# Kernel optimization log

Measured on AMD Instinct MI355X. Metric: run time of the kernel, lower is better.

## Reference

```python
import jax, jax.numpy as jnp
import numpy as np

TEMPERATURE = 0.07
ASYM_F = 1.5
ASYM_M = 0.5
N_F, N_M, D = 8192, 8192, 128


def setup_inputs() -> dict:
    key = jax.random.key(0)
    kf, km = jax.random.split(key)
    proj_f = jax.random.normal(kf, (N_F, D), dtype=jnp.float32)
    proj_m = jax.random.normal(km, (N_M, D), dtype=jnp.float32)
    # module expects L2-normalized projections
    proj_f = proj_f / jnp.linalg.norm(proj_f, axis=1, keepdims=True)
    proj_m = proj_m / jnp.linalg.norm(proj_m, axis=1, keepdims=True)
    return {"proj_f": proj_f, "proj_m": proj_m}


def _directional_loss(anchor, pos, temperature):
    # anchor: (Na, D), pos: (Np, D)
    sim_pos = jnp.einsum('ad,pd->ap', anchor, pos) / temperature        # (Na, Np)
    sim_neg = jnp.einsum('ad,bd->ab', anchor, anchor) / temperature    # (Na, Na)
    n = anchor.shape[0]
    eye = jnp.eye(n, dtype=bool)
    sim_neg = jnp.where(eye, -jnp.inf, sim_neg)  # mask self-similarity
    numerator = jax.nn.logsumexp(sim_pos, axis=1)
    # logsumexp over concat([sim_pos, sim_neg]) == logaddexp of row lses (no concat materialized)
    denominator = jnp.logaddexp(numerator, jax.nn.logsumexp(sim_neg, axis=1))
    return -jnp.mean(numerator - denominator)


def reference(proj_f, proj_m):
    loss_f2m = _directional_loss(proj_f, proj_m, TEMPERATURE)
    loss_m2f = _directional_loss(proj_m, proj_f, TEMPERATURE)
    return ASYM_F * loss_f2m + ASYM_M * loss_m2f
```

## Files before the change

### kernel.cpp

```cpp
#include <hip/hip_runtime.h>

#define NROWS 8192
#define KD    128
#define SQK1C 4.5398163f

typedef __bf16 bf16x8 __attribute__((ext_vector_type(8)));
typedef float  f32x4  __attribute__((ext_vector_type(4)));

typedef __attribute__((address_space(1))) void* gas_ptr;
typedef __attribute__((address_space(3))) void* las_ptr;

__device__ __forceinline__ unsigned short f2bf(float x) {
  unsigned int u = __builtin_bit_cast(unsigned int, x);
  unsigned int r = (u + 0x7FFFu + ((u >> 16) & 1u)) >> 16;
  return (unsigned short)r;
}

__global__ __launch_bounds__(256) void prep_kernel(const float4* __restrict__ F4,
                                                   const float4* __restrict__ M4,
                                                   ushort4* __restrict__ Fb4,
                                                   ushort4* __restrict__ Mb4,
                                                   float* __restrict__ sums) {
  int i = blockIdx.x * 256 + threadIdx.x;
  float4 f = F4[i];
  float4 m = M4[i];
  ushort4 fo, mo;
  fo.x = f2bf(f.x * SQK1C); fo.y = f2bf(f.y * SQK1C);
  fo.z = f2bf(f.z * SQK1C); fo.w = f2bf(f.w * SQK1C);
  mo.x = f2bf(m.x * SQK1C); mo.y = f2bf(m.y * SQK1C);
  mo.z = f2bf(m.z * SQK1C); mo.w = f2bf(m.w * SQK1C);
  Fb4[i] = fo;
  Mb4[i] = mo;
  if (i < 4 * NROWS) sums[i] = 0.0f;
}

__global__ __launch_bounds__(256, 3) void gemm_kernel(const unsigned short* __restrict__ Fb,
                                                      const unsigned short* __restrict__ Mb,
                                                      float* __restrict__ sums) {
  __shared__ __align__(16) unsigned short lds[2][64 * KD];

  const int bx = blockIdx.x;
  const int by = blockIdx.y;
  const int z  = blockIdx.z;

  const unsigned short* A;
  const unsigned short* B;
  float* rowsum;
  float* colsum = nullptr;
  if (z == 0)      { A = Fb; B = Mb; rowsum = sums;             colsum = sums + NROWS; }
  else if (z == 1) { A = Fb; B = Fb; rowsum = sums + 2 * NROWS; }
  else             { A = Mb; B = Mb; rowsum = sums + 3 * NROWS; }

  const int tid  = threadIdx.x;
  const int lane = tid & 63;
  const int wave = tid >> 6;
  const int wr = wave >> 1, wc = wave & 1;
  const int l15 = lane & 15, l4 = lane >> 4;

  auto stageB = [&](void* dst, const unsigned short* src) {
    #pragma unroll
    for (int i = 0; i < 4; ++i) {
      const int lin = tid * 16 + i * 4096;
      const int row = lin >> 8;
      const int sbc = (lin & 255) ^ ((row & 7) << 4);
      __builtin_amdgcn_global_load_lds((gas_ptr)((const char*)src + row * 256 + sbc),
                                       (las_ptr)((char*)dst + lin), 16, 0, 0);
    }
  };

  {
    const unsigned short* Abase = A + (size_t)by * 128 * KD;
    #pragma unroll
    for (int i = 0; i < 8; ++i) {
      const int lin = tid * 16 + i * 4096;
      const int row = lin >> 8;
      const int sbc = (lin & 255) ^ ((row & 7) << 4);
      __builtin_amdgcn_global_load_lds((gas_ptr)((const char*)Abase + row * 256 + sbc),
                                       (las_ptr)((char*)lds + lin), 16, 0, 0);
    }
  }
  __syncthreads();

  bf16x8 af[4][4];
  #pragma unroll
  for (int m = 0; m < 4; ++m) {
    const int row = wr * 64 + m * 16 + l15;
    const char* ab = (const char*)lds + row * 256;
    const int sw = (row & 7) << 4;
    #pragma unroll
    for (int k = 0; k < 4; ++k)
      af[m][k] = *(const bf16x8*)(ab + ((k * 64 + l4 * 16) ^ sw));
  }
  __syncthreads();

  float rowacc[16];
  #pragma unroll
  for (int i = 0; i < 16; ++i) rowacc[i] = 0.f;

  const unsigned short* Bbase = B + (size_t)bx * 1024 * KD;
  stageB(lds[0], Bbase);
  stageB(lds[1], Bbase + 64 * KD);
  __syncthreads();

  const int brow0 = wc * 32 + l15;
  const int bsw   = (brow0 & 7) << 4;

  for (int t = 0; t < 16; ++t) {
    const char* bb = (const char*)lds[t & 1];
    const char* pb0 = bb + brow0 * 256;

    f32x4 acc[4][2] = {};
    __builtin_amdgcn_s_setprio(1);
    #pragma unroll
    for (int k = 0; k < 4; ++k) {
      const int c = (k * 64 + l4 * 16) ^ bsw;
      bf16x8 b0 = *(const bf16x8*)(pb0 + c);
      bf16x8 b1 = *(const bf16x8*)(pb0 + 16 * 256 + c);
      #pragma unroll
      for (int m = 0; m < 4; ++m) {
        acc[m][0] = __builtin_amdgcn_mfma_f32_16x16x32_bf16(af[m][k], b0, acc[m][0], 0, 0, 0);
        acc[m][1] = __builtin_amdgcn_mfma_f32_16x16x32_bf16(af[m][k], b1, acc[m][1], 0, 0, 0);
      }
    }
    __builtin_amdgcn_s_setprio(0);

    const bool diag = (z > 0) && ((((bx << 4) + t) >> 1) == by);
    if (z == 0) {
      float ca0 = 0.f, ca1 = 0.f;
      #pragma unroll
      for (int m = 0; m < 4; ++m) {
        #pragma unroll
        for (int j = 0; j < 4; ++j) {
          float v0 = __builtin_amdgcn_exp2f(acc[m][0][j]);
          float v1 = __builtin_amdgcn_exp2f(acc[m][1][j]);
          rowacc[m * 4 + j] += v0 + v1;
          ca0 += v0; ca1 += v1;
        }
      }
      ca0 += __shfl_xor(ca0, 16);
      ca0 += __shfl_xor(ca0, 32);
      ca1 += __shfl_xor(ca1, 16);
      ca1 += __shfl_xor(ca1, 32);
      if (l4 == 0) {
        float* cp = colsum + bx * 1024 + t * 64 + wc * 32 + l15;
        unsafeAtomicAdd(cp, ca0);
        unsafeAtomicAdd(cp + 16, ca1);
      }
    } else {
      #pragma unroll
      for (int m = 0; m < 4; ++m) {
        #pragma unroll
        for (int j = 0; j < 4; ++j) {
          float v0 = __builtin_amdgcn_exp2f(acc[m][0][j]);
          float v1 = __builtin_amdgcn_exp2f(acc[m][1][j]);
          if (diag) {
            const int grow = by * 128 + wr * 64 + m * 16 + l4 * 4 + j;
            const int gcol = bx * 1024 + t * 64 + wc * 32 + l15;
            if (grow == gcol)      v0 = 0.f;
            if (grow == gcol + 16) v1 = 0.f;
          }
          rowacc[m * 4 + j] += v0 + v1;
        }
      }
    }
    __syncthreads();
    if (t < 14) stageB(lds[t & 1], Bbase + (size_t)(t + 2) * 64 * KD);
  }

  #pragma unroll
  for (int i = 0; i < 16; ++i) {
    float v = rowacc[i];
    v += __shfl_xor(v, 1);
    v += __shfl_xor(v, 2);
    v += __shfl_xor(v, 4);
    v += __shfl_xor(v, 8);
    rowacc[i] = v;
  }
  if (l15 == 0) {
    const int rbase = by * 128 + wr * 64 + l4 * 4;
    #pragma unroll
    for (int i = 0; i < 16; ++i)
      unsafeAtomicAdd(rowsum + rbase + (i >> 2) * 16 + (i & 3), rowacc[i]);
  }
}

__global__ __launch_bounds__(1024) void loss_kernel(const float* __restrict__ sums,
                                                    float* __restrict__ out) {
  const float* Spf = sums;
  const float* Spm = sums + NROWS;
  const float* Snf = sums + 2 * NROWS;
  const float* Snm = sums + 3 * NROWS;
  float accf = 0.f, accm = 0.f;
  for (int i = threadIdx.x; i < NROWS; i += 1024) {
    accf += log1pf(Snf[i] / Spf[i]);
    accm += log1pf(Snm[i] / Spm[i]);
  }
  float v = 1.5f * accf + 0.5f * accm;
  #pragma unroll
  for (int s = 1; s < 64; s <<= 1) v += __shfl_xor(v, s);
  __shared__ float red[16];
  if ((threadIdx.x & 63) == 0) red[threadIdx.x >> 6] = v;
  __syncthreads();
  if (threadIdx.x == 0) {
    float s = 0.f;
    #pragma unroll
    for (int i = 0; i < 16; ++i) s += red[i];
    out[0] = s * (1.0f / NROWS);
  }
}

extern "C" void kernel_launch(void* const* d_in, const int* in_sizes, int n_in,
                              void* d_out, int out_size, void* d_ws, size_t ws_size,
                              hipStream_t stream) {
  (void)in_sizes; (void)n_in; (void)out_size; (void)ws_size;
  const float* F = (const float*)d_in[0];
  const float* M = (const float*)d_in[1];
  float* out = (float*)d_out;

  float* sums = (float*)d_ws;
  unsigned short* Fb = (unsigned short*)((char*)d_ws + 4 * NROWS * sizeof(float));
  unsigned short* Mb = Fb + (size_t)NROWS * KD;

  prep_kernel<<<dim3(NROWS * KD / 4 / 256), dim3(256), 0, stream>>>(
      (const float4*)F, (const float4*)M, (ushort4*)Fb, (ushort4*)Mb, sums);
  gemm_kernel<<<dim3(8, 64, 3), dim3(256), 0, stream>>>(Fb, Mb, sums);
  loss_kernel<<<dim3(1), dim3(1024), 0, stream>>>(sums, out);
}
```

Baseline: 82.70 us.

## Replace direct global-to-LDS loads with register-staged prefetch pipeline

Swaps the global_load_lds path for ordinary global loads into registers that are then written to swizzled LDS, with loads issued one tile ahead of the LDS write to form a deeper prefetch. A fragments are now read directly from global memory into registers, which drops the initial LDS staging and one barrier. The first MFMA of each tile takes a zero accumulator instead of zero-initialising the array. This costs extra VGPRs for the staging registers, which may reduce occupancy at the declared 3 blocks per SM.

```diff
diff --git a/kernel.cpp b/kernel.cpp
--- a/kernel.cpp
+++ b/kernel.cpp
@@ -6,9 +6,6 @@
 
 typedef __bf16 bf16x8 __attribute__((ext_vector_type(8)));
 typedef float  f32x4  __attribute__((ext_vector_type(4)));
-
-typedef __attribute__((address_space(1))) void* gas_ptr;
-typedef __attribute__((address_space(3))) void* las_ptr;
 
 __device__ __forceinline__ unsigned short f2bf(float x) {
   unsigned int u = __builtin_bit_cast(unsigned int, x);
@@ -42,6 +39,7 @@
   const int bx = blockIdx.x;
   const int by = blockIdx.y;
   const int z  = blockIdx.z;
+  const int R  = by * 128;
 
   const unsigned short* A;
   const unsigned short* B;
@@ -57,59 +55,55 @@
   const int wr = wave >> 1, wc = wave & 1;
   const int l15 = lane & 15, l4 = lane >> 4;
 
-  auto stageB = [&](void* dst, const unsigned short* src) {
-    #pragma unroll
-    for (int i = 0; i < 4; ++i) {
-      const int lin = tid * 16 + i * 4096;
-      const int row = lin >> 8;
-      const int sbc = (lin & 255) ^ ((row & 7) << 4);
-      __builtin_amdgcn_global_load_lds((gas_ptr)((const char*)src + row * 256 + sbc),
-                                       (las_ptr)((char*)dst + lin), 16, 0, 0);
-    }
-  };
-
+  bf16x8 af[4][4];
   {
-    const unsigned short* Abase = A + (size_t)by * 128 * KD;
-    #pragma unroll
-    for (int i = 0; i < 8; ++i) {
-      const int lin = tid * 16 + i * 4096;
-      const int row = lin >> 8;
-      const int sbc = (lin & 255) ^ ((row & 7) << 4);
-      __builtin_amdgcn_global_load_lds((gas_ptr)((const char*)Abase + row * 256 + sbc),
-                                       (las_ptr)((char*)lds + lin), 16, 0, 0);
-    }
-  }
+    const unsigned short* ap = A + (size_t)(R + wr * 64 + l15) * KD + l4 * 8;
+    #pragma unroll
+    for (int m = 0; m < 4; ++m)
+      #pragma unroll
+      for (int k = 0; k < 4; ++k)
+        af[m][k] = *(const bf16x8*)(ap + (size_t)m * 16 * KD + k * 32);
+  }
+
+  const char* Bbase = (const char*)(B + (size_t)bx * 1024 * KD);
+  int swaddr[4];
+  #pragma unroll
+  for (int i = 0; i < 4; ++i) {
+    const int lin = tid * 16 + i * 4096;
+    const int row = lin >> 8;
+    swaddr[i] = row * 256 + ((lin & 255) ^ ((row & 7) << 4));
+  }
+
+  float4 sreg[4];
+#define GLOAD(t) do {                                                              \
+    const char* s_ = Bbase + (size_t)(t) * 16384;                                  \
+    _Pragma("unroll")                                                              \
+    for (int i_ = 0; i_ < 4; ++i_)                                                 \
+      sreg[i_] = *(const float4*)(s_ + tid * 16 + i_ * 4096);                      \
+  } while (0)
+#define SWRITE(buf) do {                                                           \
+    _Pragma("unroll")                                                              \
+    for (int i_ = 0; i_ < 4; ++i_)                                                 \
+      *(float4*)((char*)(buf) + swaddr[i_]) = sreg[i_];                            \
+  } while (0)
+
+  GLOAD(0); SWRITE(lds[0]);
+  GLOAD(1); SWRITE(lds[1]);
+  GLOAD(2);
   __syncthreads();
 
-  bf16x8 af[4][4];
-  #pragma unroll
-  for (int m = 0; m < 4; ++m) {
-    const int row = wr * 64 + m * 16 + l15;
-    const char* ab = (const char*)lds + row * 256;
-    const int sw = (row & 7) << 4;
-    #pragma unroll
-    for (int k = 0; k < 4; ++k)
-      af[m][k] = *(const bf16x8*)(ab + ((k * 64 + l4 * 16) ^ sw));
-  }
-  __syncthreads();
-
   float rowacc[16];
   #pragma unroll
   for (int i = 0; i < 16; ++i) rowacc[i] = 0.f;
-
-  const unsigned short* Bbase = B + (size_t)bx * 1024 * KD;
-  stageB(lds[0], Bbase);
-  stageB(lds[1], Bbase + 64 * KD);
-  __syncthreads();
 
   const int brow0 = wc * 32 + l15;
   const int bsw   = (brow0 & 7) << 4;
+  const f32x4 zero4 = {};
 
   for (int t = 0; t < 16; ++t) {
-    const char* bb = (const char*)lds[t & 1];
-    const char* pb0 = bb + brow0 * 256;
-
-    f32x4 acc[4][2] = {};
+    const char* pb0 = (const char*)lds[t & 1] + brow0 * 256;
+
+    f32x4 acc[4][2];
     __builtin_amdgcn_s_setprio(1);
     #pragma unroll
     for (int k = 0; k < 4; ++k) {
@@ -118,8 +112,10 @@
       bf16x8 b1 = *(const bf16x8*)(pb0 + 16 * 256 + c);
       #pragma unroll
       for (int m = 0; m < 4; ++m) {
-        acc[m][0] = __builtin_amdgcn_mfma_f32_16x16x32_bf16(af[m][k], b0, acc[m][0], 0, 0, 0);
-        acc[m][1] = __builtin_amdgcn_mfma_f32_16x16x32_bf16(af[m][k], b1, acc[m][1], 0, 0, 0);
+        acc[m][0] = __builtin_amdgcn_mfma_f32_16x16x32_bf16(af[m][k], b0,
+                       k ? acc[m][0] : zero4, 0, 0, 0);
+        acc[m][1] = __builtin_amdgcn_mfma_f32_16x16x32_bf16(af[m][k], b1,
+                       k ? acc[m][1] : zero4, 0, 0, 0);
       }
     }
     __builtin_amdgcn_s_setprio(0);
@@ -154,7 +150,7 @@
           float v0 = __builtin_amdgcn_exp2f(acc[m][0][j]);
           float v1 = __builtin_amdgcn_exp2f(acc[m][1][j]);
           if (diag) {
-            const int grow = by * 128 + wr * 64 + m * 16 + l4 * 4 + j;
+            const int grow = R + wr * 64 + m * 16 + l4 * 4 + j;
             const int gcol = bx * 1024 + t * 64 + wc * 32 + l15;
             if (grow == gcol)      v0 = 0.f;
             if (grow == gcol + 16) v1 = 0.f;
@@ -163,9 +159,13 @@
         }
       }
     }
+
     __syncthreads();
-    if (t < 14) stageB(lds[t & 1], Bbase + (size_t)(t + 2) * 64 * KD);
-  }
+    if (t + 2 < 16) SWRITE(lds[t & 1]);
+    if (t + 3 < 16) GLOAD(t + 3);
+  }
+#undef GLOAD
+#undef SWRITE
 
   #pragma unroll
   for (int i = 0; i < 16; ++i) {
@@ -177,7 +177,7 @@
     rowacc[i] = v;
   }
   if (l15 == 0) {
-    const int rbase = by * 128 + wr * 64 + l4 * 4;
+    const int rbase = R + wr * 64 + l4 * 4;
     #pragma unroll
     for (int i = 0; i < 16; ++i)
       unsafeAtomicAdd(rowsum + rbase + (i >> 2) * 16 + (i & 3), rowacc[i]);
```

After: 135.3 us. +63.6%, slower.
